# Kernel optimization log

Hardware: AMD Instinct MI355X
Metric: run time of the kernel (lower is better)

The kernel has to match this reference:

```python
import jax, jax.numpy as jnp
import numpy as np

B, D, E, K = 8192, 1024, 8, 2048  # tokens, dim, num_experts, k (per-expert capacity)


def setup_inputs() -> dict:
    key = jax.random.key(0)
    ks = jax.random.split(key, 5)
    x = jax.random.normal(ks[0], (B, D), dtype=jnp.float32)
    Wr = jax.random.normal(ks[1], (D, E), dtype=jnp.float32) * 0.02
    br = jnp.zeros((E,), jnp.float32)
    W1 = jax.random.normal(ks[2], (E, D, 4 * D), dtype=jnp.float32) * 0.02
    b1 = jnp.zeros((E, 4 * D), jnp.float32)
    W2 = jax.random.normal(ks[3], (E, 4 * D, D), dtype=jnp.float32) * 0.02
    b2 = jnp.zeros((E, D), jnp.float32)
    return {"x": x, "Wr": Wr, "br": br, "W1": W1, "b1": b1, "W2": W2, "b2": b2}


def _dispatch_weights(x, Wr, br):
    # Expert-choice routing: softmax over experts per token, each expert picks top-K tokens.
    gate = jax.nn.softmax(x @ Wr + br, axis=-1)          # [B, E]
    vals, idx = jax.lax.top_k(gate.T, K)                 # [E, K] each
    w = jnp.zeros((x.shape[0], E), x.dtype)
    w = w.at[idx.reshape(-1), jnp.repeat(jnp.arange(E), K)].set(vals.reshape(-1))
    # torch source builds dispatch_weights via .tolist(), detaching it from autograd
    return jax.lax.stop_gradient(w)                      # [B, E]


def reference(x, Wr, br, W1, b1, W2, b2):
    w = _dispatch_weights(x, Wr, br)                     # [B, E]
    mask = (w > 0).astype(x.dtype)                       # [B, E]
    xm = x[None, :, :] * mask.T[:, :, None]              # [E, B, D] (dense masked input, as in source)
    h = jax.nn.relu(jnp.einsum('ebd,edh->ebh', xm, W1) + b1[:, None, :])   # [E, B, 4D]
    y = jnp.einsum('ebh,ehd->ebd', h, W2) + b2[:, None, :]                 # [E, B, D]
    out = jnp.einsum('ebd,be->bd', y, w)                 # weighted combine over experts
    return out
```

## Files before the change

### kernel.cpp

```cpp
#include <hip/hip_runtime.h>
#include <hip/hip_bf16.h>

#define BTOK 8192
#define DDIM 1024
#define NEXP 8
#define KCAP 2048
#define HDIM 4096
#define MB ((size_t)1048576)

typedef __attribute__((ext_vector_type(4))) float f32x4;
typedef __attribute__((ext_vector_type(8))) short bf16x8;

__device__ __forceinline__ unsigned short f2bf(float f) {
    union { float f; unsigned u; } v; v.f = f;
    unsigned r = v.u + 0x7fffu + ((v.u >> 16) & 1u);
    return (unsigned short)(r >> 16);
}

typedef __attribute__((address_space(3))) unsigned int lds_u32;
typedef __attribute__((address_space(1))) const unsigned int glb_u32;
__device__ __forceinline__ void gl_lds16(const void* g, void* l) {
    __builtin_amdgcn_global_load_lds((glb_u32*)g, (lds_u32*)l, 16, 0, 0);
}

__global__ __launch_bounds__(256) void router_kernel(
    const float* __restrict__ x, const float* __restrict__ Wr,
    const float* __restrict__ br, float* __restrict__ gateT,
    unsigned short* __restrict__ xb) {
    __shared__ float wr_s[NEXP][DDIM];
    int t = threadIdx.x;
    for (int i = t; i < NEXP * DDIM; i += 256) {
        int e = i >> 10, d = i & 1023;
        wr_s[e][d] = Wr[d * NEXP + e];
    }
    __syncthreads();
    int wid = t >> 6, lane = t & 63;
    int b = blockIdx.x * 4 + wid;
    const float4* xr = (const float4*)(x + (size_t)b * DDIM);
    float4 xv[4];
#pragma unroll
    for (int j = 0; j < 4; j++) xv[j] = xr[j * 64 + lane];
#pragma unroll
    for (int j = 0; j < 4; j++) {
        short4 s;
        s.x = (short)f2bf(xv[j].x); s.y = (short)f2bf(xv[j].y);
        s.z = (short)f2bf(xv[j].z); s.w = (short)f2bf(xv[j].w);
        *(short4*)(xb + (size_t)b * DDIM + (j * 64 + lane) * 4) = s;
    }
    double acc[NEXP];
#pragma unroll
    for (int e = 0; e < NEXP; e++) {
        double a = 0.0;
#pragma unroll
        for (int j = 0; j < 4; j++) {
            float4 wv = ((const float4*)&wr_s[e][0])[j * 64 + lane];
            a += (double)xv[j].x * wv.x + (double)xv[j].y * wv.y
               + (double)xv[j].z * wv.z + (double)xv[j].w * wv.w;
        }
#pragma unroll
        for (int s = 1; s < 64; s <<= 1) a += __shfl_xor(a, s, 64);
        acc[e] = a + (double)br[e];
    }
    if (lane == 0) {
        double mx = acc[0];
#pragma unroll
        for (int e = 1; e < NEXP; e++) mx = fmax(mx, acc[e]);
        double p[NEXP]; double ssum = 0.0;
#pragma unroll
        for (int e = 0; e < NEXP; e++) { p[e] = exp(acc[e] - mx); ssum += p[e]; }
        double inv = 1.0 / ssum;
#pragma unroll
        for (int e = 0; e < NEXP; e++) gateT[e * BTOK + b] = (float)(p[e] * inv);
    }
}

__global__ __launch_bounds__(256) void select_kernel(
    const float* __restrict__ gateT, unsigned* __restrict__ meta) {
    int e = blockIdx.x, t = threadIdx.x;
    const float* g = gateT + e * BTOK;
    __shared__ unsigned hist[256];
    __shared__ unsigned sh_prefix;
    __shared__ int sh_rem;
    if (t == 0) { sh_prefix = 0; sh_rem = KCAP; }
    __syncthreads();
    for (int pass = 0; pass < 4; pass++) {
        int shift = 24 - pass * 8;
        hist[t] = 0;
        __syncthreads();
        unsigned pfx = sh_prefix;
        for (int i = t; i < BTOK; i += 256) {
            unsigned key = __float_as_uint(g[i]);
            if (pass == 0 || (key >> (shift + 8)) == pfx)
                atomicAdd(&hist[(key >> shift) & 255u], 1u);
        }
        __syncthreads();
        if (t == 0) {
            int rem = sh_rem, cum = 0, d = 0;
            for (int dd = 255; dd >= 0; dd--) {
                cum += (int)hist[dd];
                if (cum >= rem) { d = dd; break; }
            }
            sh_rem = rem - (cum - (int)hist[d]);
            sh_prefix = (pfx << 8) | (unsigned)d;
        }
        __syncthreads();
    }
    unsigned cutoff = sh_prefix;
    int cnt = 0;
    for (int i = t; i < BTOK; i += 256)
        if (__float_as_uint(g[i]) > cutoff) cnt++;
    __shared__ int red[256];
    red[t] = cnt; __syncthreads();
    for (int s = 128; s > 0; s >>= 1) { if (t < s) red[t] += red[t + s]; __syncthreads(); }
    if (t == 0) { meta[e] = cutoff; meta[NEXP + e] = (unsigned)red[0]; }
}

__global__ __launch_bounds__(256) void build_kernel(
    const float* __restrict__ gateT, const unsigned* __restrict__ meta,
    unsigned* __restrict__ cnt, int* __restrict__ idx_list, float* __restrict__ wt_list) {
    int e = blockIdx.y;
    int b = blockIdx.x * 256 + threadIdx.x;
    float gv = gateT[(size_t)e * BTOK + b];
    if (__float_as_uint(gv) > meta[e]) {
        unsigned pos = atomicAdd(&cnt[e], 1u);
        if (pos < KCAP) {
            idx_list[(size_t)e * KCAP + pos] = b;
            wt_list[(size_t)e * KCAP + pos] = gv;
        }
    }
}

__global__ __launch_bounds__(256) void tie_kernel(
    const float* __restrict__ gateT, const unsigned* __restrict__ meta,
    unsigned* __restrict__ cnt, int* __restrict__ idx_list, float* __restrict__ wt_list) {
    int e = blockIdx.x, t = threadIdx.x;
    unsigned cutoff = meta[e];
    int need = KCAP - (int)meta[NEXP + e];
    const float* g = gateT + (size_t)e * BTOK;
    __shared__ int pre[256];
    int base = t * 32;
    int c = 0;
    for (int j = 0; j < 32; j++) c += (__float_as_uint(g[base + j]) == cutoff) ? 1 : 0;
    pre[t] = c;
    __syncthreads();
    for (int s = 1; s < 256; s <<= 1) {
        int v = (t >= s) ? pre[t - s] : 0;
        __syncthreads();
        pre[t] += v;
        __syncthreads();
    }
    int rank = pre[t] - c;
    for (int j = 0; j < 32; j++) {
        float gv = g[base + j];
        if (__float_as_uint(gv) == cutoff) {
            if (rank < need) {
                unsigned pos = atomicAdd(&cnt[e], 1u);
                if (pos < KCAP) {
                    idx_list[(size_t)e * KCAP + pos] = base + j;
                    wt_list[(size_t)e * KCAP + pos] = gv;
                }
            }
            rank++;
        }
    }
}

__global__ __launch_bounds__(256) void invb_kernel(
    const int* __restrict__ idx_list, int* __restrict__ inv) {
    int i = blockIdx.x * 256 + threadIdx.x;
    int e = i >> 11, slot = i & (KCAP - 1);
    inv[(size_t)e * BTOK + idx_list[i]] = slot;
}

__global__ __launch_bounds__(256) void tcvt_kernel(
    const float* __restrict__ src, unsigned short* __restrict__ dst, int R, int C) {
    size_t zoff = (size_t)blockIdx.z * R * C;
    src += zoff; dst += zoff;
    __shared__ unsigned short tile[64][72];
    int c0 = blockIdx.x * 64, r0 = blockIdx.y * 64;
    int t = threadIdx.x;
    int cq = t & 15, rr = t >> 4;
#pragma unroll
    for (int ri = 0; ri < 4; ri++) {
        int r = ri * 16 + rr;
        float4 v = *(const float4*)(src + (size_t)(r0 + r) * C + c0 + cq * 4);
        tile[cq * 4 + 0][r] = f2bf(v.x);
        tile[cq * 4 + 1][r] = f2bf(v.y);
        tile[cq * 4 + 2][r] = f2bf(v.z);
        tile[cq * 4 + 3][r] = f2bf(v.w);
    }
    __syncthreads();
    int rq = t & 15, cc = t >> 4;
#pragma unroll
    for (int ci = 0; ci < 4; ci++) {
        int c = ci * 16 + cc;
        *(short4*)(dst + (size_t)(c0 + c) * R + r0 + rq * 4) = *(const short4*)&tile[c][rq * 4];
    }
}


__global__ __launch_bounds__(256) void gemm1_kernel(
    const unsigned short* __restrict__ xb, const unsigned short* __restrict__ w1t,
    const float* __restrict__ b1, const int* __restrict__ idx_list,
    unsigned short* __restrict__ h) {
    int e = blockIdx.z;
    w1t     += (size_t)e * DDIM * HDIM;
    b1      += (size_t)e * HDIM;
    idx_list += (size_t)e * KCAP;
    h       += (size_t)e * KCAP * HDIM;
    __shared__ unsigned short As[128 * 64];
    __shared__ unsigned short Bs[128 * 64];
    __shared__ int toks[128];
    int t = threadIdx.x;
    int m0 = blockIdx.x * 128, n0 = blockIdx.y * 128;
    if (t < 128) toks[t] = idx_list[m0 + t];
    __syncthreads();
    int w = t >> 6, lane = t & 63;
    int lrow8 = lane >> 3, lcol = lane & 7;
    unsigned swz = (unsigned)(((lcol ^ lrow8) & 7) << 4);
    const char* aptr[4]; const char* bptr[4];
    unsigned short* alds[4]; unsigned short* blds[4];
#pragma unroll
    for (int i = 0; i < 4; i++) {
        int rr = i * 32 + w * 8 + lrow8;
        aptr[i] = (const char*)(xb + (size_t)toks[rr] * DDIM) + swz;
        bptr[i] = (const char*)(w1t + (size_t)(n0 + rr) * DDIM) + swz;
        alds[i] = As + (i * 32 + w * 8) * 64;
        blds[i] = Bs + (i * 32 + w * 8) * 64;
    }
    f32x4 acc[4][4] = {};
    int fr = lane & 15, kg = lane >> 4;
    int wr = (w >> 1) * 64, wc = (w & 1) * 64;
    for (int kt = 0; kt < DDIM; kt += 64) {
        __syncthreads();
#pragma unroll
        for (int i = 0; i < 4; i++) {
            gl_lds16(aptr[i], alds[i]);
            gl_lds16(bptr[i], blds[i]);
            aptr[i] += 128; bptr[i] += 128;
        }
        __syncthreads();
#pragma unroll
        for (int kk = 0; kk < 2; kk++) {
            bf16x8 af[4], bf[4];
#pragma unroll
            for (int mf = 0; mf < 4; mf++) {
                int r = wr + mf * 16 + fr;
                int byte = (r * 128 + kk * 64 + kg * 16) ^ ((r & 7) << 4);
                af[mf] = *(const bf16x8*)((const char*)As + byte);
            }
#pragma unroll
            for (int nf = 0; nf < 4; nf++) {
                int r = wc + nf * 16 + fr;
                int byte = (r * 128 + kk * 64 + kg * 16) ^ ((r & 7) << 4);
                bf[nf] = *(const bf16x8*)((const char*)Bs + byte);
            }
#pragma unroll
            for (int mf = 0; mf < 4; mf++)
#pragma unroll
                for (int nf = 0; nf < 4; nf++)
                    acc[mf][nf] = __builtin_amdgcn_mfma_f32_16x16x32_bf16(
                        af[mf], bf[nf], acc[mf][nf], 0, 0, 0);
        }
    }
    int hi = lane >> 4;
#pragma unroll
    for (int nf = 0; nf < 4; nf++) {
        int col = n0 + wc + nf * 16 + fr;
        float bias = b1[col];
#pragma unroll
        for (int mf = 0; mf < 4; mf++) {
            int r0 = wr + mf * 16 + hi * 4;
#pragma unroll
            for (int r = 0; r < 4; r++) {
                float v = fmaxf(acc[mf][nf][r] + bias, 0.f);
                h[(size_t)(m0 + r0 + r) * HDIM + col] = f2bf(v);
            }
        }
    }
}

__global__ __launch_bounds__(256) void gemm2y_kernel(
    const unsigned short* __restrict__ h, const unsigned short* __restrict__ w2t,
    const float* __restrict__ b2, const float* __restrict__ wt_list,
    float* __restrict__ yb) {
    int e = blockIdx.z;
    h       += (size_t)e * KCAP * HDIM;
    w2t     += (size_t)e * DDIM * HDIM;
    b2      += (size_t)e * DDIM;
    wt_list += (size_t)e * KCAP;
    yb      += (size_t)e * KCAP * DDIM;
    __shared__ unsigned short As[128 * 64];
    __shared__ unsigned short Bs[128 * 64];
    __shared__ float wts[128];
    int t = threadIdx.x;
    int m0 = blockIdx.x * 128, n0 = blockIdx.y * 128;
    if (t < 128) wts[t] = wt_list[m0 + t];
    int w = t >> 6, lane = t & 63;
    int lrow8 = lane >> 3, lcol = lane & 7;
    unsigned swz = (unsigned)(((lcol ^ lrow8) & 7) << 4);
    const char* aptr[4]; const char* bptr[4];
    unsigned short* alds[4]; unsigned short* blds[4];
#pragma unroll
    for (int i = 0; i < 4; i++) {
        int rr = i * 32 + w * 8 + lrow8;
        aptr[i] = (const char*)(h + (size_t)(m0 + rr) * HDIM) + swz;
        bptr[i] = (const char*)(w2t + (size_t)(n0 + rr) * HDIM) + swz;
        alds[i] = As + (i * 32 + w * 8) * 64;
        blds[i] = Bs + (i * 32 + w * 8) * 64;
    }
    f32x4 acc[4][4] = {};
    int fr = lane & 15, kg = lane >> 4;
    int wr = (w >> 1) * 64, wc = (w & 1) * 64;
    for (int kt = 0; kt < HDIM; kt += 64) {
        __syncthreads();
#pragma unroll
        for (int i = 0; i < 4; i++) {
            gl_lds16(aptr[i], alds[i]);
            gl_lds16(bptr[i], blds[i]);
            aptr[i] += 128; bptr[i] += 128;
        }
        __syncthreads();
#pragma unroll
        for (int kk = 0; kk < 2; kk++) {
            bf16x8 af[4], bf[4];
#pragma unroll
            for (int mf = 0; mf < 4; mf++) {
                int r = wr + mf * 16 + fr;
                int byte = (r * 128 + kk * 64 + kg * 16) ^ ((r & 7) << 4);
                af[mf] = *(const bf16x8*)((const char*)As + byte);
            }
#pragma unroll
            for (int nf = 0; nf < 4; nf++) {
                int r = wc + nf * 16 + fr;
                int byte = (r * 128 + kk * 64 + kg * 16) ^ ((r & 7) << 4);
                bf[nf] = *(const bf16x8*)((const char*)Bs + byte);
            }
#pragma unroll
            for (int mf = 0; mf < 4; mf++)
#pragma unroll
                for (int nf = 0; nf < 4; nf++)
                    acc[mf][nf] = __builtin_amdgcn_mfma_f32_16x16x32_bf16(
                        af[mf], bf[nf], acc[mf][nf], 0, 0, 0);
        }
    }
    int hi = lane >> 4;
#pragma unroll
    for (int nf = 0; nf < 4; nf++) {
        int col = n0 + wc + nf * 16 + fr;
        float bias = b2[col];
#pragma unroll
        for (int mf = 0; mf < 4; mf++) {
            int r0 = wr + mf * 16 + hi * 4;
#pragma unroll
            for (int r = 0; r < 4; r++) {
                int lrow = r0 + r;
                yb[(size_t)(m0 + lrow) * DDIM + col] = wts[lrow] * (acc[mf][nf][r] + bias);
            }
        }
    }
}

__global__ __launch_bounds__(256) void gemm2_fb(
    const unsigned short* __restrict__ h, const unsigned short* __restrict__ w2t,
    const float* __restrict__ b2, const int* __restrict__ idx_list,
    const float* __restrict__ wt_list, float* __restrict__ out) {
    __shared__ unsigned short As[128 * 64];
    __shared__ unsigned short Bs[128 * 64];
    __shared__ int toks[128];
    __shared__ float wts[128];
    int t = threadIdx.x;
    int m0 = blockIdx.x * 128, n0 = blockIdx.y * 128;
    int z = blockIdx.z;
    if (t < 128) { toks[t] = idx_list[m0 + t]; wts[t] = wt_list[m0 + t]; }
    __syncthreads();
    int w = t >> 6, lane = t & 63;
    int lrow8 = lane >> 3, lcol = lane & 7;
    unsigned swz = (unsigned)(((lcol ^ lrow8) & 7) << 4);
    const char* aptr[4]; const char* bptr[4];
    unsigned short* alds[4]; unsigned short* blds[4];
#pragma unroll
    for (int i = 0; i < 4; i++) {
        int rr = i * 32 + w * 8 + lrow8;
        aptr[i] = (const char*)(h + (size_t)(m0 + rr) * HDIM + z * 2048) + swz;
        bptr[i] = (const char*)(w2t + (size_t)(n0 + rr) * HDIM + z * 2048) + swz;
        alds[i] = As + (i * 32 + w * 8) * 64;
        blds[i] = Bs + (i * 32 + w * 8) * 64;
    }
    f32x4 acc[4][4] = {};
    int fr = lane & 15, kg = lane >> 4;
    int wr = (w >> 1) * 64, wc = (w & 1) * 64;
    for (int kt = 0; kt < 2048; kt += 64) {
        __syncthreads();
#pragma unroll
        for (int i = 0; i < 4; i++) {
            gl_lds16(aptr[i], alds[i]);
            gl_lds16(bptr[i], blds[i]);
            aptr[i] += 128; bptr[i] += 128;
        }
        __syncthreads();
#pragma unroll
        for (int kk = 0; kk < 2; kk++) {
            bf16x8 af[4], bf[4];
#pragma unroll
            for (int mf = 0; mf < 4; mf++) {
                int r = wr + mf * 16 + fr;
                int byte = (r * 128 + kk * 64 + kg * 16) ^ ((r & 7) << 4);
                af[mf] = *(const bf16x8*)((const char*)As + byte);
            }
#pragma unroll
            for (int nf = 0; nf < 4; nf++) {
                int r = wc + nf * 16 + fr;
                int byte = (r * 128 + kk * 64 + kg * 16) ^ ((r & 7) << 4);
                bf[nf] = *(const bf16x8*)((const char*)Bs + byte);
            }
#pragma unroll
            for (int mf = 0; mf < 4; mf++)
#pragma unroll
                for (int nf = 0; nf < 4; nf++)
                    acc[mf][nf] = __builtin_amdgcn_mfma_f32_16x16x32_bf16(
                        af[mf], bf[nf], acc[mf][nf], 0, 0, 0);
        }
    }
    int hi = lane >> 4;
#pragma unroll
    for (int nf = 0; nf < 4; nf++) {
        int col = n0 + wc + nf * 16 + fr;
        float bias = (z == 0) ? b2[col] : 0.f;
#pragma unroll
        for (int mf = 0; mf < 4; mf++) {
            int r0 = wr + mf * 16 + hi * 4;
#pragma unroll
            for (int r = 0; r < 4; r++) {
                int lrow = r0 + r;
                atomicAdd(&out[(size_t)toks[lrow] * DDIM + col],
                          wts[lrow] * (acc[mf][nf][r] + bias));
            }
        }
    }
}

__global__ __launch_bounds__(256) void combine_kernel(
    const float* __restrict__ yb, const int* __restrict__ inv,
    float* __restrict__ out) {
    int b = blockIdx.x, t = threadIdx.x;
    float4 acc = {0.f, 0.f, 0.f, 0.f};
#pragma unroll
    for (int e = 0; e < NEXP; e++) {
        int s = inv[(size_t)e * BTOK + b];
        if (s >= 0) {
            float4 v = *(const float4*)(yb + ((size_t)e * KCAP + s) * DDIM + t * 4);
            acc.x += v.x; acc.y += v.y; acc.z += v.z; acc.w += v.w;
        }
    }
    *(float4*)(out + (size_t)b * DDIM + t * 4) = acc;
}

extern "C" void kernel_launch(void* const* d_in, const int* in_sizes, int n_in,
                              void* d_out, int out_size, void* d_ws, size_t ws_size,
                              hipStream_t stream) {
    const float* x  = (const float*)d_in[0];
    const float* Wr = (const float*)d_in[1];
    const float* br = (const float*)d_in[2];
    const float* W1 = (const float*)d_in[3];
    const float* b1 = (const float*)d_in[4];
    const float* W2 = (const float*)d_in[5];
    const float* b2 = (const float*)d_in[6];
    float* out = (float*)d_out;

    char* ws = (char*)d_ws;
    float*    gateT    = (float*)ws;
    unsigned* meta     = (unsigned*)(ws + 262144);
    unsigned* cnt      = meta + 16;
    int*      idx_list = (int*)(ws + 327680);
    float*    wt_list  = (float*)(ws + 393216);
    int*      inv      = (int*)(ws + 458752);
    unsigned short* xbuf = (unsigned short*)(ws + 1 * MB);

    unsigned short* w1t  = (unsigned short*)(ws + 17 * MB);
    unsigned short* w2t  = (unsigned short*)(ws + 81 * MB);
    unsigned short* hbuf = (unsigned short*)(ws + 145 * MB);
    float*          yb   = (float*)(ws + 273 * MB);
    const size_t NEED_BATCH = 337 * MB;
    unsigned short* w1t_pe = (unsigned short*)(ws + 17 * MB);
    unsigned short* w2t_pe = (unsigned short*)(ws + 25 * MB);
    unsigned short* h_pe   = (unsigned short*)(ws + 33 * MB);
    const size_t NEED_PE = 49 * MB;

    bool batched = (ws_size >= NEED_BATCH);
    if (!batched && ws_size < NEED_PE) return;

    hipMemsetAsync(cnt, 0, NEXP * sizeof(unsigned), stream);

    router_kernel<<<dim3(BTOK / 4), 256, 0, stream>>>(x, Wr, br, gateT, xbuf);
    select_kernel<<<dim3(NEXP), 256, 0, stream>>>(gateT, meta);
    build_kernel<<<dim3(BTOK / 256, NEXP), 256, 0, stream>>>(gateT, meta, cnt, idx_list, wt_list);
    tie_kernel<<<dim3(NEXP), 256, 0, stream>>>(gateT, meta, cnt, idx_list, wt_list);

    if (batched) {
        hipMemsetAsync(inv, 0xFF, (size_t)NEXP * BTOK * sizeof(int), stream);
        tcvt_kernel<<<dim3(HDIM / 64, DDIM / 64, NEXP), 256, 0, stream>>>(W1, w1t, DDIM, HDIM);
        tcvt_kernel<<<dim3(DDIM / 64, HDIM / 64, NEXP), 256, 0, stream>>>(W2, w2t, HDIM, DDIM);
        invb_kernel<<<dim3(NEXP * KCAP / 256), 256, 0, stream>>>(idx_list, inv);
        gemm1_kernel<<<dim3(KCAP / 128, HDIM / 128, NEXP), 256, 0, stream>>>(
            xbuf, w1t, b1, idx_list, hbuf);
        gemm2y_kernel<<<dim3(KCAP / 128, DDIM / 128, NEXP), 256, 0, stream>>>(
            hbuf, w2t, b2, wt_list, yb);
        combine_kernel<<<dim3(BTOK), 256, 0, stream>>>(yb, inv, out);
    } else {
        hipMemsetAsync(d_out, 0, (size_t)out_size * sizeof(float), stream);
        for (int e = 0; e < NEXP; e++) {
            tcvt_kernel<<<dim3(HDIM / 64, DDIM / 64, 1), 256, 0, stream>>>(
                W1 + (size_t)e * DDIM * HDIM, w1t_pe, DDIM, HDIM);
            gemm1_kernel<<<dim3(KCAP / 128, HDIM / 128, 1), 256, 0, stream>>>(
                xbuf, w1t_pe, b1 + (size_t)e * HDIM, idx_list + (size_t)e * KCAP, h_pe);
            tcvt_kernel<<<dim3(DDIM / 64, HDIM / 64, 1), 256, 0, stream>>>(
                W2 + (size_t)e * HDIM * DDIM, w2t_pe, HDIM, DDIM);
            gemm2_fb<<<dim3(KCAP / 128, DDIM / 128, 2), 256, 0, stream>>>(
                h_pe, w2t_pe, b2 + (size_t)e * DDIM, idx_list + (size_t)e * KCAP,
                wt_list + (size_t)e * KCAP, out);
        }
    }
}
```

Before: 626.8 us.

## Rewrite expert GEMMs with 256x256 tiles and 4-stage async LDS pipeline

Both expert GEMM kernels move from 128x128 tiles with 256 threads and a single-buffered load/sync/compute loop to 256x256 tiles with 512 threads. K is staged in 32-wide slices through a 4-slot LDS ring that is prefetched three stages ahead, with explicit vmcnt waits and s_barrier instead of two __syncthreads per step. MFMA bursts now run under raised wave priority. The per-expert fallback path and its atomic gemm2 kernel are removed, so the workspace must now be large enough for the batched path. The larger tiles cut global and LDS traffic per FLOP, but the grid shrinks (gemm2 drops to 256 blocks) and register pressure rises with the 8x4 accumulator array.

```diff
diff --git a/kernel.cpp b/kernel.cpp
--- a/kernel.cpp
+++ b/kernel.cpp
@@ -199,78 +199,82 @@
 }
 
 
-__global__ __launch_bounds__(256) void gemm1_kernel(
+#define RSLOT (256 * 32)
+
+__global__ __launch_bounds__(512, 2) void gemm1_kernel(
     const unsigned short* __restrict__ xb, const unsigned short* __restrict__ w1t,
     const float* __restrict__ b1, const int* __restrict__ idx_list,
     unsigned short* __restrict__ h) {
     int e = blockIdx.z;
-    w1t     += (size_t)e * DDIM * HDIM;
-    b1      += (size_t)e * HDIM;
+    w1t      += (size_t)e * DDIM * HDIM;
+    b1       += (size_t)e * HDIM;
     idx_list += (size_t)e * KCAP;
-    h       += (size_t)e * KCAP * HDIM;
-    __shared__ unsigned short As[128 * 64];
-    __shared__ unsigned short Bs[128 * 64];
-    __shared__ int toks[128];
+    h        += (size_t)e * KCAP * HDIM;
+    __shared__ unsigned short As[4 * RSLOT];
+    __shared__ unsigned short Bs[4 * RSLOT];
+    __shared__ int toks[256];
     int t = threadIdx.x;
-    int m0 = blockIdx.x * 128, n0 = blockIdx.y * 128;
-    if (t < 128) toks[t] = idx_list[m0 + t];
+    int m0 = blockIdx.x * 256, n0 = blockIdx.y * 256;
+    if (t < 256) toks[t] = idx_list[m0 + t];
     __syncthreads();
     int w = t >> 6, lane = t & 63;
-    int lrow8 = lane >> 3, lcol = lane & 7;
-    unsigned swz = (unsigned)(((lcol ^ lrow8) & 7) << 4);
-    const char* aptr[4]; const char* bptr[4];
-    unsigned short* alds[4]; unsigned short* blds[4];
-#pragma unroll
-    for (int i = 0; i < 4; i++) {
-        int rr = i * 32 + w * 8 + lrow8;
-        aptr[i] = (const char*)(xb + (size_t)toks[rr] * DDIM) + swz;
-        bptr[i] = (const char*)(w1t + (size_t)(n0 + rr) * DDIM) + swz;
-        alds[i] = As + (i * 32 + w * 8) * 64;
-        blds[i] = Bs + (i * 32 + w * 8) * 64;
-    }
-    f32x4 acc[4][4] = {};
+    int l2 = lane >> 2;
+    unsigned swq = (unsigned)(((lane & 3) ^ ((lane >> 3) & 3)) << 4);
+    const char* pa0 = (const char*)(xb + (size_t)toks[w * 16 + l2] * DDIM) + swq;
+    const char* pa1 = (const char*)(xb + (size_t)toks[128 + w * 16 + l2] * DDIM) + swq;
+    const char* pb0 = (const char*)(w1t + (size_t)(n0 + w * 16 + l2) * DDIM) + swq;
+    const char* pb1 = (const char*)(w1t + (size_t)(n0 + 128 + w * 16 + l2) * DDIM) + swq;
+    unsigned short* da0 = As + (w * 16) * 32;
+    unsigned short* da1 = As + (128 + w * 16) * 32;
+    unsigned short* db0 = Bs + (w * 16) * 32;
+    unsigned short* db1 = Bs + (128 + w * 16) * 32;
+#define STAGE1(slot, tt) do { size_t ko = (size_t)(tt) * 64; int so = (slot) * RSLOT; \
+    gl_lds16(pa0 + ko, da0 + so); gl_lds16(pa1 + ko, da1 + so);                        \
+    gl_lds16(pb0 + ko, db0 + so); gl_lds16(pb1 + ko, db1 + so); } while (0)
+    int wm = w >> 2, wn = w & 3;
     int fr = lane & 15, kg = lane >> 4;
-    int wr = (w >> 1) * 64, wc = (w & 1) * 64;
-    for (int kt = 0; kt < DDIM; kt += 64) {
-        __syncthreads();
-#pragma unroll
-        for (int i = 0; i < 4; i++) {
-            gl_lds16(aptr[i], alds[i]);
-            gl_lds16(bptr[i], blds[i]);
-            aptr[i] += 128; bptr[i] += 128;
-        }
-        __syncthreads();
-#pragma unroll
-        for (int kk = 0; kk < 2; kk++) {
-            bf16x8 af[4], bf[4];
-#pragma unroll
-            for (int mf = 0; mf < 4; mf++) {
-                int r = wr + mf * 16 + fr;
-                int byte = (r * 128 + kk * 64 + kg * 16) ^ ((r & 7) << 4);
-                af[mf] = *(const bf16x8*)((const char*)As + byte);
-            }
-#pragma unroll
-            for (int nf = 0; nf < 4; nf++) {
-                int r = wc + nf * 16 + fr;
-                int byte = (r * 128 + kk * 64 + kg * 16) ^ ((r & 7) << 4);
-                bf[nf] = *(const bf16x8*)((const char*)Bs + byte);
-            }
-#pragma unroll
-            for (int mf = 0; mf < 4; mf++)
-#pragma unroll
-                for (int nf = 0; nf < 4; nf++)
-                    acc[mf][nf] = __builtin_amdgcn_mfma_f32_16x16x32_bf16(
-                        af[mf], bf[nf], acc[mf][nf], 0, 0, 0);
-        }
-    }
+    unsigned koffr = (unsigned)((kg ^ ((fr >> 1) & 3)) << 4);
+    const int NT = DDIM / 32;
+    f32x4 acc[8][4] = {};
+    STAGE1(0, 0); STAGE1(1, 1); STAGE1(2, 2);
+    asm volatile("s_waitcnt vmcnt(8)" ::: "memory");
+    __builtin_amdgcn_s_barrier();
+    for (int kt = 0; kt < NT; kt++) {
+        if (kt + 3 < NT) STAGE1((kt + 3) & 3, kt + 3);
+        const char* ab = (const char*)(As + (kt & 3) * RSLOT);
+        const char* bb = (const char*)(Bs + (kt & 3) * RSLOT);
+        bf16x8 af[8], bf[4];
+#pragma unroll
+        for (int mf = 0; mf < 8; mf++)
+            af[mf] = *(const bf16x8*)(ab + (wm * 128 + mf * 16 + fr) * 64 + koffr);
+#pragma unroll
+        for (int nf = 0; nf < 4; nf++)
+            bf[nf] = *(const bf16x8*)(bb + (wn * 64 + nf * 16 + fr) * 64 + koffr);
+        __builtin_amdgcn_s_setprio(1);
+#pragma unroll
+        for (int mf = 0; mf < 8; mf++)
+#pragma unroll
+            for (int nf = 0; nf < 4; nf++)
+                acc[mf][nf] = __builtin_amdgcn_mfma_f32_16x16x32_bf16(
+                    af[mf], bf[nf], acc[mf][nf], 0, 0, 0);
+        __builtin_amdgcn_s_setprio(0);
+        if (kt + 1 < NT) {
+            int rem = NT - 2 - kt;
+            if (rem >= 2)      asm volatile("s_waitcnt vmcnt(8)" ::: "memory");
+            else if (rem == 1) asm volatile("s_waitcnt vmcnt(4)" ::: "memory");
+            else               asm volatile("s_waitcnt vmcnt(0)" ::: "memory");
+            __builtin_amdgcn_s_barrier();
+        }
+    }
+#undef STAGE1
     int hi = lane >> 4;
 #pragma unroll
     for (int nf = 0; nf < 4; nf++) {
-        int col = n0 + wc + nf * 16 + fr;
+        int col = n0 + wn * 64 + nf * 16 + fr;
         float bias = b1[col];
 #pragma unroll
-        for (int mf = 0; mf < 4; mf++) {
-            int r0 = wr + mf * 16 + hi * 4;
+        for (int mf = 0; mf < 8; mf++) {
+            int r0 = wm * 128 + mf * 16 + hi * 4;
 #pragma unroll
             for (int r = 0; r < 4; r++) {
                 float v = fmaxf(acc[mf][nf][r] + bias, 0.f);
@@ -280,7 +284,7 @@
     }
 }
 
-__global__ __launch_bounds__(256) void gemm2y_kernel(
+__global__ __launch_bounds__(512, 2) void gemm2y_kernel(
     const unsigned short* __restrict__ h, const unsigned short* __restrict__ w2t,
     const float* __restrict__ b2, const float* __restrict__ wt_list,
     float* __restrict__ yb) {
@@ -290,151 +294,75 @@
     b2      += (size_t)e * DDIM;
     wt_list += (size_t)e * KCAP;
     yb      += (size_t)e * KCAP * DDIM;
-    __shared__ unsigned short As[128 * 64];
-    __shared__ unsigned short Bs[128 * 64];
-    __shared__ float wts[128];
+    __shared__ unsigned short As[4 * RSLOT];
+    __shared__ unsigned short Bs[4 * RSLOT];
+    __shared__ float wts[256];
     int t = threadIdx.x;
-    int m0 = blockIdx.x * 128, n0 = blockIdx.y * 128;
-    if (t < 128) wts[t] = wt_list[m0 + t];
+    int m0 = blockIdx.x * 256, n0 = blockIdx.y * 256;
+    if (t < 256) wts[t] = wt_list[m0 + t];
+    __syncthreads();
     int w = t >> 6, lane = t & 63;
-    int lrow8 = lane >> 3, lcol = lane & 7;
-    unsigned swz = (unsigned)(((lcol ^ lrow8) & 7) << 4);
-    const char* aptr[4]; const char* bptr[4];
-    unsigned short* alds[4]; unsigned short* blds[4];
-#pragma unroll
-    for (int i = 0; i < 4; i++) {
-        int rr = i * 32 + w * 8 + lrow8;
-        aptr[i] = (const char*)(h + (size_t)(m0 + rr) * HDIM) + swz;
-        bptr[i] = (const char*)(w2t + (size_t)(n0 + rr) * HDIM) + swz;
-        alds[i] = As + (i * 32 + w * 8) * 64;
-        blds[i] = Bs + (i * 32 + w * 8) * 64;
-    }
-    f32x4 acc[4][4] = {};
+    int l2 = lane >> 2;
+    unsigned swq = (unsigned)(((lane & 3) ^ ((lane >> 3) & 3)) << 4);
+    const char* pa0 = (const char*)(h + (size_t)(m0 + w * 16 + l2) * HDIM) + swq;
+    const char* pa1 = (const char*)(h + (size_t)(m0 + 128 + w * 16 + l2) * HDIM) + swq;
+    const char* pb0 = (const char*)(w2t + (size_t)(n0 + w * 16 + l2) * HDIM) + swq;
+    const char* pb1 = (const char*)(w2t + (size_t)(n0 + 128 + w * 16 + l2) * HDIM) + swq;
+    unsigned short* da0 = As + (w * 16) * 32;
+    unsigned short* da1 = As + (128 + w * 16) * 32;
+    unsigned short* db0 = Bs + (w * 16) * 32;
+    unsigned short* db1 = Bs + (128 + w * 16) * 32;
+#define STAGE2(slot, tt) do { size_t ko = (size_t)(tt) * 64; int so = (slot) * RSLOT; \
+    gl_lds16(pa0 + ko, da0 + so); gl_lds16(pa1 + ko, da1 + so);                        \
+    gl_lds16(pb0 + ko, db0 + so); gl_lds16(pb1 + ko, db1 + so); } while (0)
+    int wm = w >> 2, wn = w & 3;
     int fr = lane & 15, kg = lane >> 4;
-    int wr = (w >> 1) * 64, wc = (w & 1) * 64;
-    for (int kt = 0; kt < HDIM; kt += 64) {
-        __syncthreads();
-#pragma unroll
-        for (int i = 0; i < 4; i++) {
-            gl_lds16(aptr[i], alds[i]);
-            gl_lds16(bptr[i], blds[i]);
-            aptr[i] += 128; bptr[i] += 128;
-        }
-        __syncthreads();
-#pragma unroll
-        for (int kk = 0; kk < 2; kk++) {
-            bf16x8 af[4], bf[4];
-#pragma unroll
-            for (int mf = 0; mf < 4; mf++) {
-                int r = wr + mf * 16 + fr;
-                int byte = (r * 128 + kk * 64 + kg * 16) ^ ((r & 7) << 4);
-                af[mf] = *(const bf16x8*)((const char*)As + byte);
-            }
-#pragma unroll
-            for (int nf = 0; nf < 4; nf++) {
-                int r = wc + nf * 16 + fr;
-                int byte = (r * 128 + kk * 64 + kg * 16) ^ ((r & 7) << 4);
-                bf[nf] = *(const bf16x8*)((const char*)Bs + byte);
-            }
-#pragma unroll
-            for (int mf = 0; mf < 4; mf++)
-#pragma unroll
-                for (int nf = 0; nf < 4; nf++)
-                    acc[mf][nf] = __builtin_amdgcn_mfma_f32_16x16x32_bf16(
-                        af[mf], bf[nf], acc[mf][nf], 0, 0, 0);
-        }
-    }
+    unsigned koffr = (unsigned)((kg ^ ((fr >> 1) & 3)) << 4);
+    const int NT = HDIM / 32;
+    f32x4 acc[8][4] = {};
+    STAGE2(0, 0); STAGE2(1, 1); STAGE2(2, 2);
+    asm volatile("s_waitcnt vmcnt(8)" ::: "memory");
+    __builtin_amdgcn_s_barrier();
+    for (int kt = 0; kt < NT; kt++) {
+        if (kt + 3 < NT) STAGE2((kt + 3) & 3, kt + 3);
+        const char* ab = (const char*)(As + (kt & 3) * RSLOT);
+        const char* bb = (const char*)(Bs + (kt & 3) * RSLOT);
+        bf16x8 af[8], bf[4];
+#pragma unroll
+        for (int mf = 0; mf < 8; mf++)
+            af[mf] = *(const bf16x8*)(ab + (wm * 128 + mf * 16 + fr) * 64 + koffr);
+#pragma unroll
+        for (int nf = 0; nf < 4; nf++)
+            bf[nf] = *(const bf16x8*)(bb + (wn * 64 + nf * 16 + fr) * 64 + koffr);
+        __builtin_amdgcn_s_setprio(1);
+#pragma unroll
+        for (int mf = 0; mf < 8; mf++)
+#pragma unroll
+            for (int nf = 0; nf < 4; nf++)
+                acc[mf][nf] = __builtin_amdgcn_mfma_f32_16x16x32_bf16(
+                    af[mf], bf[nf], acc[mf][nf], 0, 0, 0);
+        __builtin_amdgcn_s_setprio(0);
+        if (kt + 1 < NT) {
+            int rem = NT - 2 - kt;
+            if (rem >= 2)      asm volatile("s_waitcnt vmcnt(8)" ::: "memory");
+            else if (rem == 1) asm volatile("s_waitcnt vmcnt(4)" ::: "memory");
+            else               asm volatile("s_waitcnt vmcnt(0)" ::: "memory");
+            __builtin_amdgcn_s_barrier();
+        }
+    }
+#undef STAGE2
     int hi = lane >> 4;
 #pragma unroll
     for (int nf = 0; nf < 4; nf++) {
-        int col = n0 + wc + nf * 16 + fr;
+        int col = n0 + wn * 64 + nf * 16 + fr;
         float bias = b2[col];
 #pragma unroll
-        for (int mf = 0; mf < 4; mf++) {
-            int r0 = wr + mf * 16 + hi * 4;
+        for (int mf = 0; mf < 8; mf++) {
+            int r0 = wm * 128 + mf * 16 + hi * 4;
 #pragma unroll
             for (int r = 0; r < 4; r++) {
                 int lrow = r0 + r;
                 yb[(size_t)(m0 + lrow) * DDIM + col] = wts[lrow] * (acc[mf][nf][r] + bias);
-            }
-        }
-    }
-}
-
-__global__ __launch_bounds__(256) void gemm2_fb(
-    const unsigned short* __restrict__ h, const unsigned short* __restrict__ w2t,
-    const float* __restrict__ b2, const int* __restrict__ idx_list,
-    const float* __restrict__ wt_list, float* __restrict__ out) {
-    __shared__ unsigned short As[128 * 64];
-    __shared__ unsigned short Bs[128 * 64];
-    __shared__ int toks[128];
-    __shared__ float wts[128];
-    int t = threadIdx.x;
-    int m0 = blockIdx.x * 128, n0 = blockIdx.y * 128;
-    int z = blockIdx.z;
-    if (t < 128) { toks[t] = idx_list[m0 + t]; wts[t] = wt_list[m0 + t]; }
-    __syncthreads();
-    int w = t >> 6, lane = t & 63;
-    int lrow8 = lane >> 3, lcol = lane & 7;
-    unsigned swz = (unsigned)(((lcol ^ lrow8) & 7) << 4);
-    const char* aptr[4]; const char* bptr[4];
-    unsigned short* alds[4]; unsigned short* blds[4];
-#pragma unroll
-    for (int i = 0; i < 4; i++) {
-        int rr = i * 32 + w * 8 + lrow8;
-        aptr[i] = (const char*)(h + (size_t)(m0 + rr) * HDIM + z * 2048) + swz;
-        bptr[i] = (const char*)(w2t + (size_t)(n0 + rr) * HDIM + z * 2048) + swz;
-        alds[i] = As + (i * 32 + w * 8) * 64;
-        blds[i] = Bs + (i * 32 + w * 8) * 64;
-    }
-    f32x4 acc[4][4] = {};
-    int fr = lane & 15, kg = lane >> 4;
-    int wr = (w >> 1) * 64, wc = (w & 1) * 64;
-    for (int kt = 0; kt < 2048; kt += 64) {
-        __syncthreads();
-#pragma unroll
-        for (int i = 0; i < 4; i++) {
-            gl_lds16(aptr[i], alds[i]);
-            gl_lds16(bptr[i], blds[i]);
-            aptr[i] += 128; bptr[i] += 128;
-        }
-        __syncthreads();
-#pragma unroll
-        for (int kk = 0; kk < 2; kk++) {
-            bf16x8 af[4], bf[4];
-#pragma unroll
-            for (int mf = 0; mf < 4; mf++) {
-                int r = wr + mf * 16 + fr;
-                int byte = (r * 128 + kk * 64 + kg * 16) ^ ((r & 7) << 4);
-                af[mf] = *(const bf16x8*)((const char*)As + byte);
-            }
-#pragma unroll
-            for (int nf = 0; nf < 4; nf++) {
-                int r = wc + nf * 16 + fr;
-                int byte = (r * 128 + kk * 64 + kg * 16) ^ ((r & 7) << 4);
-                bf[nf] = *(const bf16x8*)((const char*)Bs + byte);
-            }
-#pragma unroll
-            for (int mf = 0; mf < 4; mf++)
-#pragma unroll
-                for (int nf = 0; nf < 4; nf++)
-                    acc[mf][nf] = __builtin_amdgcn_mfma_f32_16x16x32_bf16(
-                        af[mf], bf[nf], acc[mf][nf], 0, 0, 0);
-        }
-    }
-    int hi = lane >> 4;
-#pragma unroll
-    for (int nf = 0; nf < 4; nf++) {
-        int col = n0 + wc + nf * 16 + fr;
-        float bias = (z == 0) ? b2[col] : 0.f;
-#pragma unroll
-        for (int mf = 0; mf < 4; mf++) {
-            int r0 = wr + mf * 16 + hi * 4;
-#pragma unroll
-            for (int r = 0; r < 4; r++) {
-                int lrow = r0 + r;
-                atomicAdd(&out[(size_t)toks[lrow] * DDIM + col],
-                          wts[lrow] * (acc[mf][nf][r] + bias));
             }
         }
     }
@@ -476,49 +404,28 @@
     float*    wt_list  = (float*)(ws + 393216);
     int*      inv      = (int*)(ws + 458752);
     unsigned short* xbuf = (unsigned short*)(ws + 1 * MB);
-
     unsigned short* w1t  = (unsigned short*)(ws + 17 * MB);
     unsigned short* w2t  = (unsigned short*)(ws + 81 * MB);
     unsigned short* hbuf = (unsigned short*)(ws + 145 * MB);
     float*          yb   = (float*)(ws + 273 * MB);
-    const size_t NEED_BATCH = 337 * MB;
-    unsigned short* w1t_pe = (unsigned short*)(ws + 17 * MB);
-    unsigned short* w2t_pe = (unsigned short*)(ws + 25 * MB);
-    unsigned short* h_pe   = (unsigned short*)(ws + 33 * MB);
-    const size_t NEED_PE = 49 * MB;
-
-    bool batched = (ws_size >= NEED_BATCH);
-    if (!batched && ws_size < NEED_PE) return;
+    const size_t NEED = 337 * MB;
+    if (ws_size < NEED) return;
 
     hipMemsetAsync(cnt, 0, NEXP * sizeof(unsigned), stream);
+    hipMemsetAsync(inv, 0xFF, (size_t)NEXP * BTOK * sizeof(int), stream);
 
     router_kernel<<<dim3(BTOK / 4), 256, 0, stream>>>(x, Wr, br, gateT, xbuf);
     select_kernel<<<dim3(NEXP), 256, 0, stream>>>(gateT, meta);
     build_kernel<<<dim3(BTOK / 256, NEXP), 256, 0, stream>>>(gateT, meta, cnt, idx_list, wt_list);
     tie_kernel<<<dim3(NEXP), 256, 0, stream>>>(gateT, meta, cnt, idx_list, wt_list);
 
-    if (batched) {
-        hipMemsetAsync(inv, 0xFF, (size_t)NEXP * BTOK * sizeof(int), stream);
-        tcvt_kernel<<<dim3(HDIM / 64, DDIM / 64, NEXP), 256, 0, stream>>>(W1, w1t, DDIM, HDIM);
-        tcvt_kernel<<<dim3(DDIM / 64, HDIM / 64, NEXP), 256, 0, stream>>>(W2, w2t, HDIM, DDIM);
-        invb_kernel<<<dim3(NEXP * KCAP / 256), 256, 0, stream>>>(idx_list, inv);
-        gemm1_kernel<<<dim3(KCAP / 128, HDIM / 128, NEXP), 256, 0, stream>>>(
-            xbuf, w1t, b1, idx_list, hbuf);
-        gemm2y_kernel<<<dim3(KCAP / 128, DDIM / 128, NEXP), 256, 0, stream>>>(
-            hbuf, w2t, b2, wt_list, yb);
-        combine_kernel<<<dim3(BTOK), 256, 0, stream>>>(yb, inv, out);
-    } else {
-        hipMemsetAsync(d_out, 0, (size_t)out_size * sizeof(float), stream);
-        for (int e = 0; e < NEXP; e++) {
-            tcvt_kernel<<<dim3(HDIM / 64, DDIM / 64, 1), 256, 0, stream>>>(
-                W1 + (size_t)e * DDIM * HDIM, w1t_pe, DDIM, HDIM);
-            gemm1_kernel<<<dim3(KCAP / 128, HDIM / 128, 1), 256, 0, stream>>>(
-                xbuf, w1t_pe, b1 + (size_t)e * HDIM, idx_list + (size_t)e * KCAP, h_pe);
-            tcvt_kernel<<<dim3(DDIM / 64, HDIM / 64, 1), 256, 0, stream>>>(
-                W2 + (size_t)e * HDIM * DDIM, w2t_pe, HDIM, DDIM);
-            gemm2_fb<<<dim3(KCAP / 128, DDIM / 128, 2), 256, 0, stream>>>(
-                h_pe, w2t_pe, b2 + (size_t)e * DDIM, idx_list + (size_t)e * KCAP,
-                wt_list + (size_t)e * KCAP, out);
-        }
-    }
-}
+    tcvt_kernel<<<dim3(HDIM / 64, DDIM / 64, NEXP), 256, 0, stream>>>(W1, w1t, DDIM, HDIM);
+    tcvt_kernel<<<dim3(DDIM / 64, HDIM / 64, NEXP), 256, 0, stream>>>(W2, w2t, HDIM, DDIM);
+    invb_kernel<<<dim3(NEXP * KCAP / 256), 256, 0, stream>>>(idx_list, inv);
+
+    gemm1_kernel<<<dim3(KCAP / 256, HDIM / 256, NEXP), 512, 0, stream>>>(
+        xbuf, w1t, b1, idx_list, hbuf);
+    gemm2y_kernel<<<dim3(KCAP / 256, DDIM / 256, NEXP), 512, 0, stream>>>(
+        hbuf, w2t, b2, wt_list, yb);
+    combine_kernel<<<dim3(BTOK), 256, 0, stream>>>(yb, inv, out);
+}
```

After: 647.9 us. +3.4%, slower.
